# Performance work log

Hardware: AMD Instinct MI355X
Metric: run time of the kernel (lower is better)

## Reference

```python
import jax, jax.numpy as jnp
import numpy as np

N_NODES = 100000
N_EDGES = 1000000
D = 64


def _deg_inv_sqrt(idx, n):
    deg = jax.ops.segment_sum(jnp.ones(idx.shape[0], jnp.float32), idx, num_segments=n)
    deg = jnp.maximum(deg, 1.0)  # DGL clamps zero degrees to 1
    return jax.lax.rsqrt(deg)


def _graph_conv(x, W, b, src, dst, out_norm, in_norm):
    # norm='both': h = D_in^{-1/2} A D_out^{-1/2} x W + b
    h = x * out_norm[:, None]
    agg = jax.ops.segment_sum(h[src], dst, num_segments=x.shape[0])
    agg = agg * in_norm[:, None]
    return agg @ W + b


def setup_inputs() -> dict:
    key = jax.random.key(0)
    ks = jax.random.split(key, 8)
    x = jax.random.normal(ks[0], (N_NODES, D), dtype=jnp.float32)
    src = jax.random.randint(ks[1], (N_EDGES,), 0, N_NODES, dtype=jnp.int32)
    dst = jax.random.randint(ks[2], (N_EDGES,), 0, N_NODES, dtype=jnp.int32)
    s = 1.0 / np.sqrt(D)
    W1 = jax.random.normal(ks[3], (D, D), dtype=jnp.float32) * s
    W2 = jax.random.normal(ks[4], (D, D), dtype=jnp.float32) * s
    W3 = jax.random.normal(ks[5], (D, D), dtype=jnp.float32) * s
    b1 = jnp.zeros((D,), jnp.float32)
    b2 = jnp.zeros((D,), jnp.float32)
    b3 = jnp.zeros((D,), jnp.float32)
    return {"x": x, "src": src, "dst": dst,
            "W1": W1, "b1": b1, "W2": W2, "b2": b2, "W3": W3, "b3": b3}


def reference(x, src, dst, W1, b1, W2, b2, W3, b3):
    n = x.shape[0]
    out_norm = _deg_inv_sqrt(src, n)  # source out-degree norm
    in_norm = _deg_inv_sqrt(dst, n)   # dest in-degree norm
    h = _graph_conv(x, W1, b1, src, dst, out_norm, in_norm)
    h = jax.nn.relu(h)
    h = _graph_conv(h, W2, b2, src, dst, out_norm, in_norm)
    h = jax.nn.relu(h)
    h = _graph_conv(h, W3, b3, src, dst, out_norm, in_norm)
    return h
```

## Files before the change

kernel.cpp:

```cpp
#include <hip/hip_runtime.h>
#include <hip/hip_fp16.h>

#define D 64
#define SZ 512
#define EPB 2048
#define CAPB 8192

static __device__ __forceinline__ __half2 u2h2(unsigned u) {
    union { unsigned u; __half2 h; } c; c.u = u; return c.h;
}
static __device__ __forceinline__ unsigned h22u(__half2 h) {
    union { __half2 h; unsigned u; } c; c.h = h; return c.u;
}

__global__ __launch_bounds__(256) void scatter_kernel(
    const int* __restrict__ src, const int* __restrict__ dst,
    int* __restrict__ gcntD, int* __restrict__ gcntS,
    unsigned* __restrict__ packD, unsigned short* __restrict__ packS,
    int E, int nb) {
    int tid = threadIdx.x;
    __shared__ int hD[256], hS[256], baseD[256], baseS[256], curD[256], curS[256];
    __shared__ int es[EPB], ed[EPB];
    hD[tid] = 0; hS[tid] = 0; curD[tid] = 0; curS[tid] = 0;
    __syncthreads();
    int ebase = (int)blockIdx.x * EPB;
#pragma unroll
    for (int k = 0; k < EPB / 256; k++) {
        int e = ebase + k * 256 + tid;
        int s = -1, d = 0;
        if (e < E) { s = src[e]; d = dst[e]; }
        es[k * 256 + tid] = s;
        ed[k * 256 + tid] = d;
        if (s >= 0) {
            atomicAdd(&hD[d >> 9], 1);
            atomicAdd(&hS[s >> 9], 1);
        }
    }
    __syncthreads();
    if (tid < nb) {
        int c = hD[tid];
        baseD[tid] = tid * CAPB + (c ? atomicAdd(&gcntD[tid], c) : 0);
        c = hS[tid];
        baseS[tid] = tid * CAPB + (c ? atomicAdd(&gcntS[tid], c) : 0);
    }
    __syncthreads();
#pragma unroll
    for (int k = 0; k < EPB / 256; k++) {
        int s = es[k * 256 + tid];
        if (s >= 0) {
            int d = ed[k * 256 + tid];
            int bd = d >> 9, bs_ = s >> 9;
            int ld = atomicAdd(&curD[bd], 1);
            int ls = atomicAdd(&curS[bs_], 1);
            packD[baseD[bd] + ld] = ((unsigned)s << 9) | (unsigned)(d & 511);
            packS[baseS[bs_] + ls] = (unsigned short)(s & 511);
        }
    }
}

__global__ __launch_bounds__(256) void build_kernel(
    const unsigned* __restrict__ packD, const unsigned short* __restrict__ packS,
    const int* __restrict__ gcntD, const int* __restrict__ gcntS,
    int* __restrict__ csr, int* __restrict__ rowbeg, int* __restrict__ rowend,
    float* __restrict__ in_norm, float* __restrict__ out_norm,
    int n, int nb) {
    int tid = threadIdx.x;
    __shared__ int cnt[512], lptr[512], tmp[256];
    bool roleD = ((int)blockIdx.x < nb);
    int b = roleD ? (int)blockIdx.x : (int)blockIdx.x - nb;
    int bs = b * CAPB;
    int be = bs + (roleD ? gcntD[b] : gcntS[b]);
    cnt[tid] = 0; cnt[tid + 256] = 0;
    __syncthreads();
    if (roleD) {
        for (int i = bs + tid; i < be; i += 256)
            atomicAdd(&cnt[packD[i] & 511], 1);
        __syncthreads();
        int a0 = cnt[2 * tid], a1 = cnt[2 * tid + 1];
        tmp[tid] = a0 + a1; __syncthreads();
        for (int off = 1; off < 256; off <<= 1) {
            int u = (tid >= off) ? tmp[tid - off] : 0; __syncthreads();
            tmp[tid] += u; __syncthreads();
        }
        int ex = tmp[tid] - (a0 + a1);
        lptr[2 * tid] = ex; lptr[2 * tid + 1] = ex + a0;
        __syncthreads();
        int v0 = b * SZ + tid, v1 = v0 + 256;
        if (v0 < n) {
            rowbeg[v0] = bs + lptr[tid];
            rowend[v0] = bs + lptr[tid] + cnt[tid];
            in_norm[v0] = rsqrtf((float)max(cnt[tid], 1));
        }
        if (v1 < n) {
            rowbeg[v1] = bs + lptr[tid + 256];
            rowend[v1] = bs + lptr[tid + 256] + cnt[tid + 256];
            in_norm[v1] = rsqrtf((float)max(cnt[tid + 256], 1));
        }
        __syncthreads();
        for (int i = bs + tid; i < be; i += 256) {
            unsigned p = packD[i];
            int slot = atomicAdd(&lptr[p & 511], 1);
            csr[bs + slot] = (int)(p >> 9);
        }
    } else {
        for (int i = bs + tid; i < be; i += 256)
            atomicAdd(&cnt[packS[i]], 1);
        __syncthreads();
        int v0 = b * SZ + tid, v1 = v0 + 256;
        if (v0 < n) out_norm[v0] = rsqrtf((float)max(cnt[tid], 1));
        if (v1 < n) out_norm[v1] = rsqrtf((float)max(cnt[tid + 256], 1));
    }
}

__global__ __launch_bounds__(256, 4) void gemm_kernel(
    const float* __restrict__ X, const float* __restrict__ W,
    const float* __restrict__ scale, __half* __restrict__ P, int n) {
    __shared__ float Ws[64 * 64];
    __shared__ float Xs[64 * 64];
    int tid = threadIdx.x;
    int row0 = (int)blockIdx.x * 64;
    if (row0 >= n) return;
    {
        const float4* W4 = (const float4*)W;
        float4* Ws4 = (float4*)Ws;
#pragma unroll
        for (int i = 0; i < 4; i++) Ws4[tid + 256 * i] = W4[tid + 256 * i];
    }
    {
#pragma unroll
        for (int i = 0; i < 4; i++) {
            int idx = tid + 256 * i;
            int r = idx >> 4, kq = idx & 15;
            float4 v = make_float4(0.f, 0.f, 0.f, 0.f);
            int row = row0 + r;
            if (row < n) v = ((const float4*)X)[(size_t)row * 16 + kq];
            *(float4*)&Xs[r * 64 + ((kq ^ (r & 15)) << 2)] = v;
        }
    }
    __syncthreads();

    int tx = tid & 15, ty = tid >> 4;
    float acc[4][4] = {};
#pragma unroll 4
    for (int kc = 0; kc < 16; kc++) {
        float4 wv[4];
#pragma unroll
        for (int j = 0; j < 4; j++) wv[j] = *(float4*)&Ws[(4 * kc + j) * 64 + 4 * tx];
#pragma unroll
        for (int r = 0; r < 4; r++) {
            int row = 4 * ty + r;
            float4 xv = *(float4*)&Xs[row * 64 + ((kc ^ (row & 15)) << 2)];
            acc[r][0] = fmaf(xv.x, wv[0].x, acc[r][0]);
            acc[r][1] = fmaf(xv.x, wv[0].y, acc[r][1]);
            acc[r][2] = fmaf(xv.x, wv[0].z, acc[r][2]);
            acc[r][3] = fmaf(xv.x, wv[0].w, acc[r][3]);
            acc[r][0] = fmaf(xv.y, wv[1].x, acc[r][0]);
            acc[r][1] = fmaf(xv.y, wv[1].y, acc[r][1]);
            acc[r][2] = fmaf(xv.y, wv[1].z, acc[r][2]);
            acc[r][3] = fmaf(xv.y, wv[1].w, acc[r][3]);
            acc[r][0] = fmaf(xv.z, wv[2].x, acc[r][0]);
            acc[r][1] = fmaf(xv.z, wv[2].y, acc[r][1]);
            acc[r][2] = fmaf(xv.z, wv[2].z, acc[r][2]);
            acc[r][3] = fmaf(xv.z, wv[2].w, acc[r][3]);
            acc[r][0] = fmaf(xv.w, wv[3].x, acc[r][0]);
            acc[r][1] = fmaf(xv.w, wv[3].y, acc[r][1]);
            acc[r][2] = fmaf(xv.w, wv[3].z, acc[r][2]);
            acc[r][3] = fmaf(xv.w, wv[3].w, acc[r][3]);
        }
    }
#pragma unroll
    for (int r = 0; r < 4; r++) {
        int row = row0 + 4 * ty + r;
        if (row < n) {
            float sc = scale[row];
            uint2 o;
            o.x = h22u(__floats2half2_rn(acc[r][0] * sc, acc[r][1] * sc));
            o.y = h22u(__floats2half2_rn(acc[r][2] * sc, acc[r][3] * sc));
            *(uint2*)&P[(size_t)row * 64 + 4 * tx] = o;
        }
    }
}

__global__ __launch_bounds__(256) void gather_gemm_kernel(
    const uint4* __restrict__ P4, const int* __restrict__ csr,
    const int* __restrict__ rowbeg, const int* __restrict__ rowend,
    const float* __restrict__ in_norm, const float* __restrict__ out_norm,
    const float* __restrict__ bias, const float* __restrict__ W,
    __half* __restrict__ Pout, int n) {
    __shared__ float Ws[64 * 64];
    int tid = threadIdx.x;
    {
        const float4* W4 = (const float4*)W;
        float4* Ws4 = (float4*)Ws;
#pragma unroll
        for (int i = 0; i < 4; i++) Ws4[tid + 256 * i] = W4[tid + 256 * i];
    }
    __syncthreads();

    int g = tid & 7;
    int base_lane = tid & 56;
    int v = (int)blockIdx.x * 32 + (tid >> 3);
    if (v >= n) return;

    int begin = rowbeg[v];
    int end = rowend[v];
    float al0 = 0.f, al1 = 0.f, al2 = 0.f, al3 = 0.f;
    float ah0 = 0.f, ah1 = 0.f, ah2 = 0.f, ah3 = 0.f;
    for (int e = begin; e < end; e += 8) {
        int ee = e + g;
        int jl = (ee < end) ? csr[ee] : -1;
        int js[8];
#pragma unroll
        for (int k = 0; k < 8; k++) js[k] = __shfl(jl, base_lane + k, 64);
        uint4 t[8];
#pragma unroll
        for (int k = 0; k < 8; k++) {
            t[k] = make_uint4(0u, 0u, 0u, 0u);
            if (js[k] >= 0) t[k] = P4[(size_t)js[k] * 8 + g];
        }
#pragma unroll
        for (int k = 0; k < 8; k++) {
            float2 f0 = __half22float2(u2h2(t[k].x));
            float2 f1 = __half22float2(u2h2(t[k].y));
            float2 f2 = __half22float2(u2h2(t[k].z));
            float2 f3 = __half22float2(u2h2(t[k].w));
            al0 += f0.x; al1 += f0.y; al2 += f1.x; al3 += f1.y;
            ah0 += f2.x; ah1 += f2.y; ah2 += f3.x; ah3 += f3.y;
        }
    }
    float inv = in_norm[v];
    float sc = out_norm[v];
    float4 blo = ((const float4*)bias)[2 * g];
    float4 bhi = ((const float4*)bias)[2 * g + 1];
    float hr[8];
    hr[0] = fmaxf(fmaf(al0, inv, blo.x), 0.f) * sc;
    hr[1] = fmaxf(fmaf(al1, inv, blo.y), 0.f) * sc;
    hr[2] = fmaxf(fmaf(al2, inv, blo.z), 0.f) * sc;
    hr[3] = fmaxf(fmaf(al3, inv, blo.w), 0.f) * sc;
    hr[4] = fmaxf(fmaf(ah0, inv, bhi.x), 0.f) * sc;
    hr[5] = fmaxf(fmaf(ah1, inv, bhi.y), 0.f) * sc;
    hr[6] = fmaxf(fmaf(ah2, inv, bhi.z), 0.f) * sc;
    hr[7] = fmaxf(fmaf(ah3, inv, bhi.w), 0.f) * sc;

    float o[8];
#pragma unroll
    for (int i = 0; i < 8; i++) o[i] = 0.f;
#pragma unroll
    for (int gp = 0; gp < 8; gp++) {
#pragma unroll
        for (int ip = 0; ip < 8; ip++) {
            float hk = __shfl(hr[ip], base_lane + gp, 64);
            const float* wrow = &Ws[(8 * gp + ip) * 64 + 8 * g];
            float4 w0 = *(const float4*)wrow;
            float4 w1 = *(const float4*)(wrow + 4);
            o[0] = fmaf(hk, w0.x, o[0]); o[1] = fmaf(hk, w0.y, o[1]);
            o[2] = fmaf(hk, w0.z, o[2]); o[3] = fmaf(hk, w0.w, o[3]);
            o[4] = fmaf(hk, w1.x, o[4]); o[5] = fmaf(hk, w1.y, o[5]);
            o[6] = fmaf(hk, w1.z, o[6]); o[7] = fmaf(hk, w1.w, o[7]);
        }
    }
    uint4 t;
    t.x = h22u(__floats2half2_rn(o[0], o[1]));
    t.y = h22u(__floats2half2_rn(o[2], o[3]));
    t.z = h22u(__floats2half2_rn(o[4], o[5]));
    t.w = h22u(__floats2half2_rn(o[6], o[7]));
    ((uint4*)Pout)[(size_t)v * 8 + g] = t;
}

__global__ __launch_bounds__(256) void gather_kernel(
    const uint4* __restrict__ P4, const int* __restrict__ csr,
    const int* __restrict__ rowbeg, const int* __restrict__ rowend,
    const float* __restrict__ in_norm, const float* __restrict__ bias,
    float4* __restrict__ out4, int n) {
    int tid = threadIdx.x;
    int g = tid & 7;
    int base_lane = tid & 56;
    int v = blockIdx.x * 32 + (tid >> 3);
    if (v >= n) return;

    int begin = rowbeg[v];
    int end = rowend[v];
    float inv = in_norm[v];
    float4 blo = ((const float4*)bias)[2 * g];
    float4 bhi = ((const float4*)bias)[2 * g + 1];

    float al0 = 0.f, al1 = 0.f, al2 = 0.f, al3 = 0.f;
    float ah0 = 0.f, ah1 = 0.f, ah2 = 0.f, ah3 = 0.f;

    for (int e = begin; e < end; e += 8) {
        int ee = e + g;
        int jl = (ee < end) ? csr[ee] : -1;
        int js[8];
#pragma unroll
        for (int k = 0; k < 8; k++) js[k] = __shfl(jl, base_lane + k, 64);
        uint4 t[8];
#pragma unroll
        for (int k = 0; k < 8; k++) {
            t[k] = make_uint4(0u, 0u, 0u, 0u);
            if (js[k] >= 0) t[k] = P4[(size_t)js[k] * 8 + g];
        }
#pragma unroll
        for (int k = 0; k < 8; k++) {
            float2 f0 = __half22float2(u2h2(t[k].x));
            float2 f1 = __half22float2(u2h2(t[k].y));
            float2 f2 = __half22float2(u2h2(t[k].z));
            float2 f3 = __half22float2(u2h2(t[k].w));
            al0 += f0.x; al1 += f0.y; al2 += f1.x; al3 += f1.y;
            ah0 += f2.x; ah1 += f2.y; ah2 += f3.x; ah3 += f3.y;
        }
    }

    float4 o0, o1;
    o0.x = fmaf(al0, inv, blo.x); o0.y = fmaf(al1, inv, blo.y);
    o0.z = fmaf(al2, inv, blo.z); o0.w = fmaf(al3, inv, blo.w);
    o1.x = fmaf(ah0, inv, bhi.x); o1.y = fmaf(ah1, inv, bhi.y);
    o1.z = fmaf(ah2, inv, bhi.z); o1.w = fmaf(ah3, inv, bhi.w);
    out4[(size_t)v * 16 + 2 * g] = o0;
    out4[(size_t)v * 16 + 2 * g + 1] = o1;
}


extern "C" void kernel_launch(void* const* d_in, const int* in_sizes, int n_in,
                              void* d_out, int out_size, void* d_ws, size_t ws_size,
                              hipStream_t stream) {
    const float* x  = (const float*)d_in[0];
    const int* src  = (const int*)d_in[1];
    const int* dst  = (const int*)d_in[2];
    const float* W1 = (const float*)d_in[3];
    const float* b1 = (const float*)d_in[4];
    const float* W2 = (const float*)d_in[5];
    const float* b2 = (const float*)d_in[6];
    const float* W3 = (const float*)d_in[7];
    const float* b3 = (const float*)d_in[8];

    const int N = in_sizes[0] / D;
    const int E = in_sizes[1];
    const int nb = (N + SZ - 1) / SZ;
    const int hb = (E + EPB - 1) / EPB;

    char* ws = (char*)d_ws;
    size_t off = 0;
    auto alloc = [&](size_t bytes) -> void* {
        void* p = (void*)(ws + off);
        off += (bytes + 15) & ~(size_t)15;
        return p;
    };
    int* gcntD = (int*)alloc(256 * 4);
    int* gcntS = (int*)alloc(256 * 4);
    unsigned* packD       = (unsigned*)alloc((size_t)nb * CAPB * 4);
    unsigned short* packS = (unsigned short*)alloc((size_t)nb * CAPB * 2);
    int* csr     = (int*)alloc((size_t)nb * CAPB * 4);
    int* rowbeg  = (int*)alloc((size_t)N * 4);
    int* rowend  = (int*)alloc((size_t)N * 4);
    float* innrm = (float*)alloc((size_t)N * 4);
    float* outnrm= (float*)alloc((size_t)N * 4);
    __half* bufPa = (__half*)alloc((size_t)N * D * 2);
    __half* bufPb = (__half*)alloc((size_t)N * D * 2);

    const int gemmb = (N + 63) / 64;
    const int sgrid = (N + 31) / 32;

    hipMemsetAsync(gcntD, 0, 2 * 256 * sizeof(int), stream);

    scatter_kernel<<<hb, 256, 0, stream>>>(src, dst, gcntD, gcntS,
                                           packD, packS, E, nb);
    build_kernel<<<2 * nb, 256, 0, stream>>>(packD, packS, gcntD, gcntS, csr,
                                             rowbeg, rowend, innrm, outnrm, N, nb);

    gemm_kernel<<<gemmb, 256, 0, stream>>>(x, W1, outnrm, bufPa, N);
    gather_gemm_kernel<<<sgrid, 256, 0, stream>>>((const uint4*)bufPa, csr, rowbeg,
                                                  rowend, innrm, outnrm, b1, W2,
                                                  bufPb, N);
    gather_gemm_kernel<<<sgrid, 256, 0, stream>>>((const uint4*)bufPb, csr, rowbeg,
                                                  rowend, innrm, outnrm, b2, W3,
                                                  bufPa, N);
    gather_kernel<<<sgrid, 256, 0, stream>>>((const uint4*)bufPa, csr, rowbeg,
                                             rowend, innrm, b3, (float4*)d_out, N);
}
```

Measured before the change: 235.0 us.

## Use 16 lanes per node in gathers with csr prefetch and vectorized scatter/build

The gather kernels now assign 16 lanes per destination node, each loading 8 bytes of features, so 16 neighbor rows are in flight per iteration. The next chunk of CSR indices is prefetched before the accumulation step, and the fused 64x64 GEMM is rewritten to match the 4-column-per-lane layout. The scatter and build kernels read edges with vectorized 16-byte loads and drop the shared staging arrays, which cuts load instructions and LDS traffic. The trade-off is half as many nodes per block, more shuffles, and more live registers for the 16 outstanding loads.

```diff
diff --git a/kernel.cpp b/kernel.cpp
--- a/kernel.cpp
+++ b/kernel.cpp
@@ -20,22 +20,30 @@
     int E, int nb) {
     int tid = threadIdx.x;
     __shared__ int hD[256], hS[256], baseD[256], baseS[256], curD[256], curS[256];
-    __shared__ int es[EPB], ed[EPB];
     hD[tid] = 0; hS[tid] = 0; curD[tid] = 0; curS[tid] = 0;
     __syncthreads();
-    int ebase = (int)blockIdx.x * EPB;
-#pragma unroll
-    for (int k = 0; k < EPB / 256; k++) {
-        int e = ebase + k * 256 + tid;
-        int s = -1, d = 0;
-        if (e < E) { s = src[e]; d = dst[e]; }
-        es[k * 256 + tid] = s;
-        ed[k * 256 + tid] = d;
-        if (s >= 0) {
-            atomicAdd(&hD[d >> 9], 1);
-            atomicAdd(&hS[s >> 9], 1);
-        }
-    }
+    int base = (int)blockIdx.x * EPB + 8 * tid;
+    int s0,s1,s2,s3,s4,s5,s6,s7, d0,d1,d2,d3,d4,d5,d6,d7;
+    if (base + 8 <= E) {
+        int4 a = *(const int4*)&src[base], b = *(const int4*)&src[base + 4];
+        s0=a.x; s1=a.y; s2=a.z; s3=a.w; s4=b.x; s5=b.y; s6=b.z; s7=b.w;
+        a = *(const int4*)&dst[base]; b = *(const int4*)&dst[base + 4];
+        d0=a.x; d1=a.y; d2=a.z; d3=a.w; d4=b.x; d5=b.y; d6=b.z; d7=b.w;
+    } else {
+        s0=s1=s2=s3=s4=s5=s6=s7=-1; d0=d1=d2=d3=d4=d5=d6=d7=0;
+        if (base + 0 < E) { s0 = src[base + 0]; d0 = dst[base + 0]; }
+        if (base + 1 < E) { s1 = src[base + 1]; d1 = dst[base + 1]; }
+        if (base + 2 < E) { s2 = src[base + 2]; d2 = dst[base + 2]; }
+        if (base + 3 < E) { s3 = src[base + 3]; d3 = dst[base + 3]; }
+        if (base + 4 < E) { s4 = src[base + 4]; d4 = dst[base + 4]; }
+        if (base + 5 < E) { s5 = src[base + 5]; d5 = dst[base + 5]; }
+        if (base + 6 < E) { s6 = src[base + 6]; d6 = dst[base + 6]; }
+        if (base + 7 < E) { s7 = src[base + 7]; d7 = dst[base + 7]; }
+    }
+#define HIST(S, Dd) if (S >= 0) { atomicAdd(&hD[Dd >> 9], 1); atomicAdd(&hS[S >> 9], 1); }
+    HIST(s0,d0) HIST(s1,d1) HIST(s2,d2) HIST(s3,d3)
+    HIST(s4,d4) HIST(s5,d5) HIST(s6,d6) HIST(s7,d7)
+#undef HIST
     __syncthreads();
     if (tid < nb) {
         int c = hD[tid];
@@ -44,18 +52,15 @@
         baseS[tid] = tid * CAPB + (c ? atomicAdd(&gcntS[tid], c) : 0);
     }
     __syncthreads();
-#pragma unroll
-    for (int k = 0; k < EPB / 256; k++) {
-        int s = es[k * 256 + tid];
-        if (s >= 0) {
-            int d = ed[k * 256 + tid];
-            int bd = d >> 9, bs_ = s >> 9;
-            int ld = atomicAdd(&curD[bd], 1);
-            int ls = atomicAdd(&curS[bs_], 1);
-            packD[baseD[bd] + ld] = ((unsigned)s << 9) | (unsigned)(d & 511);
-            packS[baseS[bs_] + ls] = (unsigned short)(s & 511);
-        }
-    }
+#define SCAT(S, Dd) if (S >= 0) { \
+        int bd = Dd >> 9, bs_ = S >> 9; \
+        int ld = atomicAdd(&curD[bd], 1); \
+        int ls = atomicAdd(&curS[bs_], 1); \
+        packD[baseD[bd] + ld] = ((unsigned)S << 9) | (unsigned)(Dd & 511); \
+        packS[baseS[bs_] + ls] = (unsigned short)(S & 511); }
+    SCAT(s0,d0) SCAT(s1,d1) SCAT(s2,d2) SCAT(s3,d3)
+    SCAT(s4,d4) SCAT(s5,d5) SCAT(s6,d6) SCAT(s7,d7)
+#undef SCAT
 }
 
 __global__ __launch_bounds__(256) void build_kernel(
@@ -73,8 +78,15 @@
     cnt[tid] = 0; cnt[tid + 256] = 0;
     __syncthreads();
     if (roleD) {
-        for (int i = bs + tid; i < be; i += 256)
-            atomicAdd(&cnt[packD[i] & 511], 1);
+        for (int i = bs + 4 * tid; i < be; i += 1024) {
+            if (i + 4 <= be) {
+                uint4 p = *(const uint4*)&packD[i];
+                atomicAdd(&cnt[p.x & 511], 1); atomicAdd(&cnt[p.y & 511], 1);
+                atomicAdd(&cnt[p.z & 511], 1); atomicAdd(&cnt[p.w & 511], 1);
+            } else {
+                for (int q = i; q < be; q++) atomicAdd(&cnt[packD[q] & 511], 1);
+            }
+        }
         __syncthreads();
         int a0 = cnt[2 * tid], a1 = cnt[2 * tid + 1];
         tmp[tid] = a0 + a1; __syncthreads();
@@ -97,14 +109,34 @@
             in_norm[v1] = rsqrtf((float)max(cnt[tid + 256], 1));
         }
         __syncthreads();
-        for (int i = bs + tid; i < be; i += 256) {
-            unsigned p = packD[i];
-            int slot = atomicAdd(&lptr[p & 511], 1);
-            csr[bs + slot] = (int)(p >> 9);
+        for (int i = bs + 4 * tid; i < be; i += 1024) {
+            if (i + 4 <= be) {
+                uint4 p = *(const uint4*)&packD[i];
+                int sl;
+                sl = atomicAdd(&lptr[p.x & 511], 1); csr[bs + sl] = (int)(p.x >> 9);
+                sl = atomicAdd(&lptr[p.y & 511], 1); csr[bs + sl] = (int)(p.y >> 9);
+                sl = atomicAdd(&lptr[p.z & 511], 1); csr[bs + sl] = (int)(p.z >> 9);
+                sl = atomicAdd(&lptr[p.w & 511], 1); csr[bs + sl] = (int)(p.w >> 9);
+            } else {
+                for (int q = i; q < be; q++) {
+                    unsigned p = packD[q];
+                    int sl = atomicAdd(&lptr[p & 511], 1);
+                    csr[bs + sl] = (int)(p >> 9);
+                }
+            }
         }
     } else {
-        for (int i = bs + tid; i < be; i += 256)
-            atomicAdd(&cnt[packS[i]], 1);
+        for (int i = bs + 8 * tid; i < be; i += 2048) {
+            if (i + 8 <= be) {
+                uint4 p = *(const uint4*)&packS[i];
+                atomicAdd(&cnt[p.x & 0xFFFF], 1); atomicAdd(&cnt[p.x >> 16], 1);
+                atomicAdd(&cnt[p.y & 0xFFFF], 1); atomicAdd(&cnt[p.y >> 16], 1);
+                atomicAdd(&cnt[p.z & 0xFFFF], 1); atomicAdd(&cnt[p.z >> 16], 1);
+                atomicAdd(&cnt[p.w & 0xFFFF], 1); atomicAdd(&cnt[p.w >> 16], 1);
+            } else {
+                for (int q = i; q < be; q++) atomicAdd(&cnt[packS[q]], 1);
+            }
+        }
         __syncthreads();
         int v0 = b * SZ + tid, v1 = v0 + 256;
         if (v0 < n) out_norm[v0] = rsqrtf((float)max(cnt[tid], 1));
@@ -197,74 +229,69 @@
     }
     __syncthreads();
 
-    int g = tid & 7;
-    int base_lane = tid & 56;
-    int v = (int)blockIdx.x * 32 + (tid >> 3);
+    int g = tid & 15;
+    int base_lane = tid & 48;
+    int v = (int)blockIdx.x * 16 + (tid >> 4);
     if (v >= n) return;
 
+    const uint2* P2 = (const uint2*)P4;
     int begin = rowbeg[v];
     int end = rowend[v];
-    float al0 = 0.f, al1 = 0.f, al2 = 0.f, al3 = 0.f;
-    float ah0 = 0.f, ah1 = 0.f, ah2 = 0.f, ah3 = 0.f;
-    for (int e = begin; e < end; e += 8) {
-        int ee = e + g;
-        int jl = (ee < end) ? csr[ee] : -1;
-        int js[8];
-#pragma unroll
-        for (int k = 0; k < 8; k++) js[k] = __shfl(jl, base_lane + k, 64);
-        uint4 t[8];
-#pragma unroll
-        for (int k = 0; k < 8; k++) {
-            t[k] = make_uint4(0u, 0u, 0u, 0u);
-            if (js[k] >= 0) t[k] = P4[(size_t)js[k] * 8 + g];
-        }
-#pragma unroll
-        for (int k = 0; k < 8; k++) {
+    float a0 = 0.f, a1 = 0.f, a2 = 0.f, a3 = 0.f;
+
+    int jl = (begin + g < end) ? csr[begin + g] : -1;
+    for (int e = begin; e < end; ) {
+        int js[16];
+#pragma unroll
+        for (int k = 0; k < 16; k++) js[k] = __shfl(jl, base_lane + k, 64);
+        uint2 t[16];
+#pragma unroll
+        for (int k = 0; k < 16; k++) {
+            t[k] = make_uint2(0u, 0u);
+            if (js[k] >= 0) t[k] = P2[(size_t)js[k] * 16 + g];
+        }
+        e += 16;
+        jl = (e + g < end) ? csr[e + g] : -1;
+#pragma unroll
+        for (int k = 0; k < 16; k++) {
             float2 f0 = __half22float2(u2h2(t[k].x));
             float2 f1 = __half22float2(u2h2(t[k].y));
-            float2 f2 = __half22float2(u2h2(t[k].z));
-            float2 f3 = __half22float2(u2h2(t[k].w));
-            al0 += f0.x; al1 += f0.y; al2 += f1.x; al3 += f1.y;
-            ah0 += f2.x; ah1 += f2.y; ah2 += f3.x; ah3 += f3.y;
+            a0 += f0.x; a1 += f0.y; a2 += f1.x; a3 += f1.y;
         }
     }
     float inv = in_norm[v];
     float sc = out_norm[v];
-    float4 blo = ((const float4*)bias)[2 * g];
-    float4 bhi = ((const float4*)bias)[2 * g + 1];
-    float hr[8];
-    hr[0] = fmaxf(fmaf(al0, inv, blo.x), 0.f) * sc;
-    hr[1] = fmaxf(fmaf(al1, inv, blo.y), 0.f) * sc;
-    hr[2] = fmaxf(fmaf(al2, inv, blo.z), 0.f) * sc;
-    hr[3] = fmaxf(fmaf(al3, inv, blo.w), 0.f) * sc;
-    hr[4] = fmaxf(fmaf(ah0, inv, bhi.x), 0.f) * sc;
-    hr[5] = fmaxf(fmaf(ah1, inv, bhi.y), 0.f) * sc;
-    hr[6] = fmaxf(fmaf(ah2, inv, bhi.z), 0.f) * sc;
-    hr[7] = fmaxf(fmaf(ah3, inv, bhi.w), 0.f) * sc;
-
-    float o[8];
-#pragma unroll
-    for (int i = 0; i < 8; i++) o[i] = 0.f;
-#pragma unroll
-    for (int gp = 0; gp < 8; gp++) {
-#pragma unroll
-        for (int ip = 0; ip < 8; ip++) {
-            float hk = __shfl(hr[ip], base_lane + gp, 64);
-            const float* wrow = &Ws[(8 * gp + ip) * 64 + 8 * g];
-            float4 w0 = *(const float4*)wrow;
-            float4 w1 = *(const float4*)(wrow + 4);
-            o[0] = fmaf(hk, w0.x, o[0]); o[1] = fmaf(hk, w0.y, o[1]);
-            o[2] = fmaf(hk, w0.z, o[2]); o[3] = fmaf(hk, w0.w, o[3]);
-            o[4] = fmaf(hk, w1.x, o[4]); o[5] = fmaf(hk, w1.y, o[5]);
-            o[6] = fmaf(hk, w1.z, o[6]); o[7] = fmaf(hk, w1.w, o[7]);
-        }
-    }
-    uint4 t;
-    t.x = h22u(__floats2half2_rn(o[0], o[1]));
-    t.y = h22u(__floats2half2_rn(o[2], o[3]));
-    t.z = h22u(__floats2half2_rn(o[4], o[5]));
-    t.w = h22u(__floats2half2_rn(o[6], o[7]));
-    ((uint4*)Pout)[(size_t)v * 8 + g] = t;
+    float4 bq = ((const float4*)bias)[g];
+    float hr0 = fmaxf(fmaf(a0, inv, bq.x), 0.f) * sc;
+    float hr1 = fmaxf(fmaf(a1, inv, bq.y), 0.f) * sc;
+    float hr2 = fmaxf(fmaf(a2, inv, bq.z), 0.f) * sc;
+    float hr3 = fmaxf(fmaf(a3, inv, bq.w), 0.f) * sc;
+
+    float o0 = 0.f, o1 = 0.f, o2 = 0.f, o3 = 0.f;
+#pragma unroll
+    for (int gp = 0; gp < 16; gp++) {
+        float h0 = __shfl(hr0, base_lane + gp, 64);
+        float h1 = __shfl(hr1, base_lane + gp, 64);
+        float h2 = __shfl(hr2, base_lane + gp, 64);
+        float h3 = __shfl(hr3, base_lane + gp, 64);
+        const float* wr = &Ws[(4 * gp) * 64 + 4 * g];
+        float4 w0 = *(const float4*)(wr);
+        float4 w1 = *(const float4*)(wr + 64);
+        float4 w2 = *(const float4*)(wr + 128);
+        float4 w3 = *(const float4*)(wr + 192);
+        o0 = fmaf(h0, w0.x, o0); o1 = fmaf(h0, w0.y, o1);
+        o2 = fmaf(h0, w0.z, o2); o3 = fmaf(h0, w0.w, o3);
+        o0 = fmaf(h1, w1.x, o0); o1 = fmaf(h1, w1.y, o1);
+        o2 = fmaf(h1, w1.z, o2); o3 = fmaf(h1, w1.w, o3);
+        o0 = fmaf(h2, w2.x, o0); o1 = fmaf(h2, w2.y, o1);
+        o2 = fmaf(h2, w2.z, o2); o3 = fmaf(h2, w2.w, o3);
+        o0 = fmaf(h3, w3.x, o0); o1 = fmaf(h3, w3.y, o1);
+        o2 = fmaf(h3, w3.z, o2); o3 = fmaf(h3, w3.w, o3);
+    }
+    uint2 t;
+    t.x = h22u(__floats2half2_rn(o0, o1));
+    t.y = h22u(__floats2half2_rn(o2, o3));
+    ((uint2*)Pout)[(size_t)v * 16 + g] = t;
 }
 
 __global__ __launch_bounds__(256) void gather_kernel(
@@ -273,50 +300,44 @@
     const float* __restrict__ in_norm, const float* __restrict__ bias,
     float4* __restrict__ out4, int n) {
     int tid = threadIdx.x;
-    int g = tid & 7;
-    int base_lane = tid & 56;
-    int v = blockIdx.x * 32 + (tid >> 3);
+    int g = tid & 15;
+    int base_lane = tid & 48;
+    int v = (int)blockIdx.x * 16 + (tid >> 4);
     if (v >= n) return;
 
+    const uint2* P2 = (const uint2*)P4;
     int begin = rowbeg[v];
     int end = rowend[v];
-    float inv = in_norm[v];
-    float4 blo = ((const float4*)bias)[2 * g];
-    float4 bhi = ((const float4*)bias)[2 * g + 1];
-
-    float al0 = 0.f, al1 = 0.f, al2 = 0.f, al3 = 0.f;
-    float ah0 = 0.f, ah1 = 0.f, ah2 = 0.f, ah3 = 0.f;
-
-    for (int e = begin; e < end; e += 8) {
-        int ee = e + g;
-        int jl = (ee < end) ? csr[ee] : -1;
-        int js[8];
-#pragma unroll
-        for (int k = 0; k < 8; k++) js[k] = __shfl(jl, base_lane + k, 64);
-        uint4 t[8];
-#pragma unroll
-        for (int k = 0; k < 8; k++) {
-            t[k] = make_uint4(0u, 0u, 0u, 0u);
-            if (js[k] >= 0) t[k] = P4[(size_t)js[k] * 8 + g];
-        }
-#pragma unroll
-        for (int k = 0; k < 8; k++) {
+    float a0 = 0.f, a1 = 0.f, a2 = 0.f, a3 = 0.f;
+
+    int jl = (begin + g < end) ? csr[begin + g] : -1;
+    for (int e = begin; e < end; ) {
+        int js[16];
+#pragma unroll
+        for (int k = 0; k < 16; k++) js[k] = __shfl(jl, base_lane + k, 64);
+        uint2 t[16];
+#pragma unroll
+        for (int k = 0; k < 16; k++) {
+            t[k] = make_uint2(0u, 0u);
+            if (js[k] >= 0) t[k] = P2[(size_t)js[k] * 16 + g];
+        }
+        e += 16;
+        jl = (e + g < end) ? csr[e + g] : -1;
+#pragma unroll
+        for (int k = 0; k < 16; k++) {
             float2 f0 = __half22float2(u2h2(t[k].x));
             float2 f1 = __half22float2(u2h2(t[k].y));
-            float2 f2 = __half22float2(u2h2(t[k].z));
-            float2 f3 = __half22float2(u2h2(t[k].w));
-            al0 += f0.x; al1 += f0.y; al2 += f1.x; al3 += f1.y;
-            ah0 += f2.x; ah1 += f2.y; ah2 += f3.x; ah3 += f3.y;
-        }
-    }
-
-    float4 o0, o1;
-    o0.x = fmaf(al0, inv, blo.x); o0.y = fmaf(al1, inv, blo.y);
-    o0.z = fmaf(al2, inv, blo.z); o0.w = fmaf(al3, inv, blo.w);
-    o1.x = fmaf(ah0, inv, bhi.x); o1.y = fmaf(ah1, inv, bhi.y);
-    o1.z = fmaf(ah2, inv, bhi.z); o1.w = fmaf(ah3, inv, bhi.w);
-    out4[(size_t)v * 16 + 2 * g] = o0;
-    out4[(size_t)v * 16 + 2 * g + 1] = o1;
+            a0 += f0.x; a1 += f0.y; a2 += f1.x; a3 += f1.y;
+        }
+    }
+    float inv = in_norm[v];
+    float4 bq = ((const float4*)bias)[g];
+    float4 o;
+    o.x = fmaf(a0, inv, bq.x);
+    o.y = fmaf(a1, inv, bq.y);
+    o.z = fmaf(a2, inv, bq.z);
+    o.w = fmaf(a3, inv, bq.w);
+    out4[(size_t)v * 16 + g] = o;
 }
 
 
@@ -358,7 +379,7 @@
     __half* bufPb = (__half*)alloc((size_t)N * D * 2);
 
     const int gemmb = (N + 63) / 64;
-    const int sgrid = (N + 31) / 32;
+    const int sgrid = (N + 15) / 16;
 
     hipMemsetAsync(gcntD, 0, 2 * 256 * sizeof(int), stream);
 
```

New measurement: 239.9 us. 2.1% more time.
